# Kernel optimization log

Hardware: AMD Instinct MI355X
Metric: run time of the kernel (lower is better)

## Reference

```python
import jax, jax.numpy as jnp
import numpy as np

B, C_IN, H, W = 8, 64, 256, 256
C_OUT, K, GROUPS, REP_DIM = 64, 3, 64, 512


def setup_inputs() -> dict:
    key = jax.random.key(0)
    k1, k2, k3 = jax.random.split(key, 3)
    x = jax.random.normal(k1, (B, C_IN, H, W), dtype=jnp.float32)
    representation = jax.random.normal(k2, (B, REP_DIM), dtype=jnp.float32)
    # Linear(representation_dim -> out_channels*k*k, bias=False) weight, [out_features, in_features]
    w_key = jax.random.normal(k3, (C_OUT * K * K, REP_DIM), dtype=jnp.float32) * (REP_DIM ** -0.5)
    return {"x": x, "representation": representation, "w_key": w_key}


def reference(x, representation, w_key):
    b = x.shape[0]
    fpg = C_IN // GROUPS          # features_per_group (input channels per group)
    opg = C_OUT // GROUPS         # output channels per group
    pad = K // 2

    # compress_key: Linear (no bias) + LeakyReLU(0.1)
    # per-sample dynamic kernels: [b, out_channels, k, k] (the repeat_interleave in the
    # original just copies this single spatial kernel across all fpg in-channels of a group)
    kern = jax.nn.leaky_relu(representation @ w_key.T, negative_slope=0.1)
    kern = kern.reshape(b, GROUPS, opg, K, K)

    # reflection pad (matches torch ReflectionPad2d)
    xp = jnp.pad(x, ((0, 0), (0, 0), (pad, pad), (pad, pad)), mode='reflect')

    # since each output channel's kernel is identical across its group's in-channels,
    # conv(sum of group channels) == sum of convs: pre-sum in-channels per group
    xg = xp.reshape(b, GROUPS, fpg, H + 2 * pad, W + 2 * pad).sum(axis=2)  # [b,g,hp,wp]

    # accumulate over the K*K kernel taps (small fixed loop), fully vectorized over b,g,h,w
    out = jnp.zeros((b, GROUPS, opg, H, W), dtype=x.dtype)
    for dy in range(K):
        for dx in range(K):
            out = out + jnp.einsum('bghw,bgo->bgohw',
                                   xg[:, :, dy:dy + H, dx:dx + W],
                                   kern[:, :, :, dy, dx])
    return out.reshape(b, C_OUT, H, W)
```

## Files before the change

kernel.cpp:

```cpp
#include <hip/hip_runtime.h>

#define B_  8
#define C_  64
#define H_  256
#define W_  256
#define REP_ 512

__global__ __launch_bounds__(256) void compute_kern_k(const float* __restrict__ rep,
                                                      const float* __restrict__ wkey,
                                                      float* __restrict__ kern) {
    int wave = blockIdx.x * 4 + (threadIdx.x >> 6);
    int lane = threadIdx.x & 63;
    int b = wave / 576;
    int o = wave - b * 576;
    const float* wrow = wkey + (size_t)o * REP_;
    const float* rrow = rep  + (size_t)b * REP_;
    float acc = 0.f;
#pragma unroll
    for (int i = 0; i < REP_ / 64; ++i) {
        int r = lane + i * 64;
        acc += rrow[r] * wrow[r];
    }
#pragma unroll
    for (int off = 32; off > 0; off >>= 1)
        acc += __shfl_xor(acc, off, 64);
    if (lane == 0) {
        float v = acc;
        kern[wave] = v > 0.f ? v : 0.1f * v;
    }
}

__global__ __launch_bounds__(256) void dwconv3x3_reflect(const float* __restrict__ x,
                                                         const float* __restrict__ kern,
                                                         float* __restrict__ out) {
    int plane = blockIdx.x >> 6;
    int rb    = blockIdx.x & 63;
    int h  = rb * 4 + (threadIdx.x >> 6);
    int c4 = (threadIdx.x & 63) << 2;

    const float* pin = x + (size_t)plane * (H_ * W_);
    const float* kp  = kern + plane * 9;
    float k[9];
#pragma unroll
    for (int i = 0; i < 9; ++i) k[i] = kp[i];

    int rows[3];
    rows[0] = (h == 0)      ? 1      : h - 1;
    rows[1] = h;
    rows[2] = (h == H_ - 1) ? H_ - 2 : h + 1;

    int li = (c4 == 0)       ? 1      : c4 - 1;
    int ri = (c4 == W_ - 4)  ? W_ - 2 : c4 + 4;

    float v[3][6];
#pragma unroll
    for (int r = 0; r < 3; ++r) {
        const float* rowp = pin + rows[r] * W_;
        float4 mid = *(const float4*)(rowp + c4);
        v[r][1] = mid.x; v[r][2] = mid.y; v[r][3] = mid.z; v[r][4] = mid.w;
        v[r][0] = rowp[li];
        v[r][5] = rowp[ri];
    }

    float4 o4;
    float* op = (float*)&o4;
#pragma unroll
    for (int j = 0; j < 4; ++j) {
        float s = 0.f;
#pragma unroll
        for (int dy = 0; dy < 3; ++dy)
#pragma unroll
            for (int dx = 0; dx < 3; ++dx)
                s += k[dy * 3 + dx] * v[dy][j + dx];
        op[j] = s;
    }
    *(float4*)(out + (size_t)plane * (H_ * W_) + h * W_ + c4) = o4;
}

extern "C" void kernel_launch(void* const* d_in, const int* in_sizes, int n_in,
                              void* d_out, int out_size, void* d_ws, size_t ws_size,
                              hipStream_t stream) {
    const float* x    = (const float*)d_in[0];
    const float* rep  = (const float*)d_in[1];
    const float* wkey = (const float*)d_in[2];
    float* out  = (float*)d_out;
    float* kern = (float*)d_ws;

    compute_kern_k<<<1152, 256, 0, stream>>>(rep, wkey, kern);
    dwconv3x3_reflect<<<32768, 256, 0, stream>>>(x, kern, out);
}
```

Measured before the change: 264.8 us.

## Process 16-row strips per wave with rolling row buffer and shuffle halos

Each wave now walks down 16 consecutive output rows and keeps a rolling 4-row register window, so every input row is loaded once per strip instead of three times. The left and right halo pixels come from neighbouring lanes through wavefront shuffles rather than extra scalar global loads. The grid drops from 32768 to 2048 blocks, which reduces parallelism and makes each thread run a longer serial loop.

```diff
diff --git a/kernel.cpp b/kernel.cpp
--- a/kernel.cpp
+++ b/kernel.cpp
@@ -30,51 +30,56 @@
     }
 }
 
-__global__ __launch_bounds__(256) void dwconv3x3_reflect(const float* __restrict__ x,
-                                                         const float* __restrict__ kern,
-                                                         float* __restrict__ out) {
-    int plane = blockIdx.x >> 6;
-    int rb    = blockIdx.x & 63;
-    int h  = rb * 4 + (threadIdx.x >> 6);
-    int c4 = (threadIdx.x & 63) << 2;
+__global__ __launch_bounds__(256) void dwconv3x3_strip(const float* __restrict__ x,
+                                                       const float* __restrict__ kern,
+                                                       float* __restrict__ out) {
+    int plane   = blockIdx.x >> 2;
+    int quarter = blockIdx.x & 3;
+    int wv   = threadIdx.x >> 6;
+    int lane = threadIdx.x & 63;
+    int r0 = quarter * 64 + wv * 16;
+    int c4 = lane << 2;
 
-    const float* pin = x + (size_t)plane * (H_ * W_);
-    const float* kp  = kern + plane * 9;
+    const float* pin  = x   + (size_t)plane * (H_ * W_);
+    float*       pout = out + (size_t)plane * (H_ * W_);
+    const float* kp   = kern + plane * 9;
     float k[9];
 #pragma unroll
     for (int i = 0; i < 9; ++i) k[i] = kp[i];
 
-    int rows[3];
-    rows[0] = (h == 0)      ? 1      : h - 1;
-    rows[1] = h;
-    rows[2] = (h == H_ - 1) ? H_ - 2 : h + 1;
+    float a[4][6];
 
-    int li = (c4 == 0)       ? 1      : c4 - 1;
-    int ri = (c4 == W_ - 4)  ? W_ - 2 : c4 + 4;
+    auto loadRow = [&](int t, float* dst) {
+        int rr = (t < 0) ? -t : ((t >= H_) ? (2 * H_ - 2 - t) : t);
+        const float* rowp = pin + rr * W_;
+        float4 m = *(const float4*)(rowp + c4);
+        dst[1] = m.x; dst[2] = m.y; dst[3] = m.z; dst[4] = m.w;
+        float lv = __shfl(m.w, lane - 1, 64);
+        dst[0] = (lane == 0) ? m.y : lv;
+        float rv = __shfl(m.x, lane + 1, 64);
+        dst[5] = (lane == 63) ? m.z : rv;
+    };
 
-    float v[3][6];
+    loadRow(r0 - 1, a[0]);
+    loadRow(r0,     a[1]);
+    loadRow(r0 + 1, a[2]);
+
 #pragma unroll
-    for (int r = 0; r < 3; ++r) {
-        const float* rowp = pin + rows[r] * W_;
-        float4 mid = *(const float4*)(rowp + c4);
-        v[r][1] = mid.x; v[r][2] = mid.y; v[r][3] = mid.z; v[r][4] = mid.w;
-        v[r][0] = rowp[li];
-        v[r][5] = rowp[ri];
+    for (int j = 0; j < 16; ++j) {
+        if (j < 15) loadRow(r0 + j + 2, a[(j + 3) & 3]);
+        const float* rm1 = a[j & 3];
+        const float* rc  = a[(j + 1) & 3];
+        const float* rp1 = a[(j + 2) & 3];
+        float4 o4;
+        float* op = (float*)&o4;
+#pragma unroll
+        for (int t = 0; t < 4; ++t) {
+            op[t] = k[0] * rm1[t] + k[1] * rm1[t + 1] + k[2] * rm1[t + 2]
+                  + k[3] * rc[t]  + k[4] * rc[t + 1]  + k[5] * rc[t + 2]
+                  + k[6] * rp1[t] + k[7] * rp1[t + 1] + k[8] * rp1[t + 2];
+        }
+        *(float4*)(pout + (size_t)(r0 + j) * W_ + c4) = o4;
     }
-
-    float4 o4;
-    float* op = (float*)&o4;
-#pragma unroll
-    for (int j = 0; j < 4; ++j) {
-        float s = 0.f;
-#pragma unroll
-        for (int dy = 0; dy < 3; ++dy)
-#pragma unroll
-            for (int dx = 0; dx < 3; ++dx)
-                s += k[dy * 3 + dx] * v[dy][j + dx];
-        op[j] = s;
-    }
-    *(float4*)(out + (size_t)plane * (H_ * W_) + h * W_ + c4) = o4;
 }
 
 extern "C" void kernel_launch(void* const* d_in, const int* in_sizes, int n_in,
@@ -87,5 +92,5 @@
     float* kern = (float*)d_ws;
 
     compute_kern_k<<<1152, 256, 0, stream>>>(rep, wkey, kern);
-    dwconv3x3_reflect<<<32768, 256, 0, stream>>>(x, kern, out);
+    dwconv3x3_strip<<<2048, 256, 0, stream>>>(x, kern, out);
 }
```

New measurement: 239.7 us. 1.1x faster.
